# Kernel tuning notes

Hardware: AMD Instinct MI355X
Metric: run time of the kernel (lower is better)

## Reference

```python
import jax, jax.numpy as jnp
import numpy as np

DEPTH = 4
HEADS = 8
DIM = 512
HID = 1024  # int(512 * 2.0)
P = 16
IMG = 224
GRID = IMG // P          # 14
NPATCH = GRID * GRID     # 196
NTOK = NPATCH + 1        # 197 (cls token)
BATCH = 64
EPS = 1e-5               # torch LayerNorm default


def layernorm(x, w, b):
    mu = jnp.mean(x, axis=-1, keepdims=True)
    var = jnp.mean(jnp.square(x - mu), axis=-1, keepdims=True)
    return (x - mu) * jax.lax.rsqrt(var + EPS) * w + b


def setup_inputs() -> dict:
    key = jax.random.key(0)
    ks = jax.random.split(key, 12)
    s = 0.02
    inp = {
        "x": jax.random.normal(ks[0], (BATCH, 3, IMG, IMG), jnp.float32),
        # patch-embed conv as matmul: kernel flattened in torch order (c, kh, kw)
        "conv_w": jax.random.normal(ks[1], (3 * P * P, DIM), jnp.float32) * s,
        "conv_b": jnp.zeros((DIM,), jnp.float32),
        "cls_token": jax.random.normal(ks[2], (1, 1, DIM), jnp.float32) * s,
        "pos_embed": jax.random.normal(ks[3], (1, NTOK, DIM), jnp.float32) * s,
        # per-block params stacked along depth
        "ln1_w": jnp.ones((DEPTH, DIM), jnp.float32),
        "ln1_b": jnp.zeros((DEPTH, DIM), jnp.float32),
        "qkv_w": jax.random.normal(ks[4], (DEPTH, DIM, 3 * DIM), jnp.float32) * s,
        "qkv_b": jnp.zeros((DEPTH, 3 * DIM), jnp.float32),
        "proj_w": jax.random.normal(ks[5], (DEPTH, DIM, DIM), jnp.float32) * s,
        "proj_b": jnp.zeros((DEPTH, DIM), jnp.float32),
        "ln2_w": jnp.ones((DEPTH, DIM), jnp.float32),
        "ln2_b": jnp.zeros((DEPTH, DIM), jnp.float32),
        "fc1_w": jax.random.normal(ks[6], (DEPTH, DIM, HID), jnp.float32) * s,
        "fc1_b": jnp.zeros((DEPTH, HID), jnp.float32),
        "fc2_w": jax.random.normal(ks[7], (DEPTH, HID, DIM), jnp.float32) * s,
        "fc2_b": jnp.zeros((DEPTH, DIM), jnp.float32),
        "norm_w": jnp.ones((DIM,), jnp.float32),
        "norm_b": jnp.zeros((DIM,), jnp.float32),
    }
    return inp


def reference(x, conv_w, conv_b, cls_token, pos_embed,
              ln1_w, ln1_b, qkv_w, qkv_b, proj_w, proj_b,
              ln2_w, ln2_b, fc1_w, fc1_b, fc2_w, fc2_b,
              norm_w, norm_b):
    B = x.shape[0]
    hd = DIM // HEADS
    scale = hd ** -0.5
    # PatchEmbed: conv with kernel=stride=patch == patch extraction + matmul
    patches = x.reshape(B, 3, GRID, P, GRID, P)
    patches = patches.transpose(0, 2, 4, 1, 3, 5).reshape(B, NPATCH, 3 * P * P)
    tok = patches @ conv_w + conv_b                      # [B, 196, DIM]
    cls = jnp.broadcast_to(cls_token, (B, 1, DIM))
    h = jnp.concatenate([cls, tok], axis=1) + pos_embed  # [B, 197, DIM]
    for i in range(DEPTH):
        # Attention block (eval mode: dropouts are identity)
        y = layernorm(h, ln1_w[i], ln1_b[i])
        qkv = (y @ qkv_w[i] + qkv_b[i]).reshape(B, NTOK, 3, HEADS, hd)
        qkv = qkv.transpose(2, 0, 3, 1, 4)               # [3, B, H, N, hd]
        q, k, v = qkv[0], qkv[1], qkv[2]
        attn = jax.nn.softmax(jnp.einsum('bhnd,bhmd->bhnm', q, k) * scale, axis=-1)
        o = jnp.einsum('bhnm,bhmd->bhnd', attn, v)
        o = o.transpose(0, 2, 1, 3).reshape(B, NTOK, DIM)
        h = h + (o @ proj_w[i] + proj_b[i])
        # MLP block (exact GELU as in torch nn.GELU)
        y = layernorm(h, ln2_w[i], ln2_b[i])
        y = jax.nn.gelu(y @ fc1_w[i] + fc1_b[i], approximate=False)
        h = h + (y @ fc2_w[i] + fc2_b[i])
    return layernorm(h, norm_w, norm_b)
```

## Files before the change

### kernel.cpp

```cpp
#include <hip/hip_runtime.h>
#include <hip/hip_bf16.h>

#define HEADS 8
#define DIM 512
#define HID 1024
#define NTOK 197
#define NPATCH 196
#define BATCH 64
#define MTOK (BATCH*NTOK)
#define MPATCH (BATCH*NPATCH)
#define KPATCH 768

typedef __attribute__((ext_vector_type(8))) short vbf8;
typedef __attribute__((ext_vector_type(4))) float vf4;

__device__ inline float bf2f(short u) {
  union { unsigned int i; float f; } v; v.i = ((unsigned int)(unsigned short)u) << 16; return v.f;
}
__device__ inline short f2bf(float f) {
  union { float f; unsigned int i; } u; u.f = f;
  unsigned int r = u.i + 0x7fffu + ((u.i >> 16) & 1u);
  return (short)(r >> 16);
}

__device__ inline void gl_lds16(const void* g, void* l) {
  __builtin_amdgcn_global_load_lds(
      (const __attribute__((address_space(1))) void*)g,
      (__attribute__((address_space(3))) void*)l, 16, 0, 0);
}

__global__ void k_cvt_t(const float* __restrict__ in, short* __restrict__ out, int K, int N) {
  int slice = blockIdx.z;
  in  += (size_t)slice * K * N;
  out += (size_t)slice * K * N;
  __shared__ short tile[64][72];
  int t = threadIdx.x;
  int k0 = blockIdx.y * 64, n0 = blockIdx.x * 64;
  int r = t >> 2, c4 = (t & 3) << 4;
  #pragma unroll
  for (int j = 0; j < 16; j += 4) {
    float4 v = *(const float4*)(in + (size_t)(k0 + r) * N + n0 + c4 + j);
    tile[r][c4 + j + 0] = f2bf(v.x);
    tile[r][c4 + j + 1] = f2bf(v.y);
    tile[r][c4 + j + 2] = f2bf(v.z);
    tile[r][c4 + j + 3] = f2bf(v.w);
  }
  __syncthreads();
  int n = t >> 2, kc = (t & 3) << 4;
  vbf8 a, b;
  #pragma unroll
  for (int j = 0; j < 8; ++j) a[j] = tile[kc + j][n];
  #pragma unroll
  for (int j = 0; j < 8; ++j) b[j] = tile[kc + 8 + j][n];
  *(vbf8*)(out + (size_t)(n0 + n) * K + k0 + kc) = a;
  *(vbf8*)(out + (size_t)(n0 + n) * K + k0 + kc + 8) = b;
}

__global__ void k_im2col(const float* __restrict__ x, short* __restrict__ patches) {
  int tid = blockIdx.x * 256 + threadIdx.x;
  if (tid >= MPATCH * 48) return;
  int b = tid / (NPATCH * 48);
  int r = tid % (NPATCH * 48);
  int p = r / 48;
  int ck = r % 48;
  int c = ck >> 4, kh = ck & 15;
  int gy = p / 14, gx = p % 14;
  const float* src = x + ((size_t)((b * 3 + c) * 224) + gy * 16 + kh) * 224 + gx * 16;
  short* dst = patches + (size_t)(b * NPATCH + p) * KPATCH + c * 256 + kh * 16;
  float4 v0 = *(const float4*)(src);
  float4 v1 = *(const float4*)(src + 4);
  float4 v2 = *(const float4*)(src + 8);
  float4 v3 = *(const float4*)(src + 12);
  vbf8 o0, o1;
  o0[0]=f2bf(v0.x); o0[1]=f2bf(v0.y); o0[2]=f2bf(v0.z); o0[3]=f2bf(v0.w);
  o0[4]=f2bf(v1.x); o0[5]=f2bf(v1.y); o0[6]=f2bf(v1.z); o0[7]=f2bf(v1.w);
  o1[0]=f2bf(v2.x); o1[1]=f2bf(v2.y); o1[2]=f2bf(v2.z); o1[3]=f2bf(v2.w);
  o1[4]=f2bf(v3.x); o1[5]=f2bf(v3.y); o1[6]=f2bf(v3.z); o1[7]=f2bf(v3.w);
  *(vbf8*)dst = o0;
  *(vbf8*)(dst + 8) = o1;
}

__global__ void k_cls(const float* __restrict__ cls, const float* __restrict__ pos,
                      float* __restrict__ h) {
  int b = blockIdx.x, t = threadIdx.x;
  float* hr = h + (size_t)b * NTOK * DIM;
  hr[t]       = cls[t]       + pos[t];
  hr[t + 256] = cls[t + 256] + pos[t + 256];
}

template<int OUTBF>
__global__ __launch_bounds__(256) void k_ln(const float* __restrict__ x,
                                            const float* __restrict__ w,
                                            const float* __restrict__ b,
                                            void* __restrict__ out) {
  int wid = threadIdx.x >> 6, lane = threadIdx.x & 63;
  int row = blockIdx.x * 4 + wid;
  const float* xr = x + (size_t)row * DIM + lane * 8;
  float4 va = *(const float4*)xr;
  float4 vb = *(const float4*)(xr + 4);
  float s  = va.x + va.y + va.z + va.w + vb.x + vb.y + vb.z + vb.w;
  float ss = va.x*va.x + va.y*va.y + va.z*va.z + va.w*va.w
           + vb.x*vb.x + vb.y*vb.y + vb.z*vb.z + vb.w*vb.w;
  #pragma unroll
  for (int o = 32; o > 0; o >>= 1) { s += __shfl_xor(s, o); ss += __shfl_xor(ss, o); }
  float mu = s * (1.0f / DIM);
  float var = ss * (1.0f / DIM) - mu * mu;
  float rs = rsqrtf(var + 1e-5f);
  float4 wa = *(const float4*)(w + lane * 8);
  float4 wb = *(const float4*)(w + lane * 8 + 4);
  float4 ba = *(const float4*)(b + lane * 8);
  float4 bb = *(const float4*)(b + lane * 8 + 4);
  float y0 = (va.x - mu) * rs * wa.x + ba.x;
  float y1 = (va.y - mu) * rs * wa.y + ba.y;
  float y2 = (va.z - mu) * rs * wa.z + ba.z;
  float y3 = (va.w - mu) * rs * wa.w + ba.w;
  float y4 = (vb.x - mu) * rs * wb.x + bb.x;
  float y5 = (vb.y - mu) * rs * wb.y + bb.y;
  float y6 = (vb.z - mu) * rs * wb.z + bb.z;
  float y7 = (vb.w - mu) * rs * wb.w + bb.w;
  if (OUTBF) {
    vbf8 pk;
    pk[0]=f2bf(y0); pk[1]=f2bf(y1); pk[2]=f2bf(y2); pk[3]=f2bf(y3);
    pk[4]=f2bf(y4); pk[5]=f2bf(y5); pk[6]=f2bf(y6); pk[7]=f2bf(y7);
    *(vbf8*)((short*)out + (size_t)row * DIM + lane * 8) = pk;
  } else {
    float4 oa, ob;
    oa.x=y0; oa.y=y1; oa.z=y2; oa.w=y3;
    ob.x=y4; ob.y=y5; ob.z=y6; ob.w=y7;
    float* op = (float*)out + (size_t)row * DIM + lane * 8;
    *(float4*)op = oa;
    *(float4*)(op + 4) = ob;
  }
}

template<int MODE, int KU>
__global__ __launch_bounds__(256) void k_gemm(
    const short* __restrict__ A, const short* __restrict__ Bt,
    const float* __restrict__ bias, void* __restrict__ out,
    const float* __restrict__ extra, int M, int N, int K)
{
  __shared__ short As[KU][128 * 64];
  __shared__ short Bs[KU][128 * 64];
  int gx = gridDim.x;
  int nwg = gx * gridDim.y;
  int orig = blockIdx.y * gx + blockIdx.x;
  int q = nwg >> 3, r = nwg & 7, xcd = orig & 7, off = orig >> 3;
  int nid = (xcd < r ? xcd * (q + 1) : r * (q + 1) + (xcd - r) * q) + off;
  int bm = nid / gx, bn = nid % gx;

  int t = threadIdx.x, wid = t >> 6, lane = t & 63;
  int wm = wid >> 1, wn = wid & 1;
  int lr = lane & 15, lk = lane >> 4;
  int srow = lane >> 3;
  int scol = (lane & 7) * 8;
  vf4 acc[4][4];
  #pragma unroll
  for (int i = 0; i < 4; ++i)
    #pragma unroll
    for (int j = 0; j < 4; ++j) {
      acc[i][j][0] = 0.f; acc[i][j][1] = 0.f; acc[i][j][2] = 0.f; acc[i][j][3] = 0.f;
    }

  const short* Abase = A  + (size_t)(bm * 128 + srow) * K + scol;
  const short* Bbase = Bt + (size_t)(bn * 128 + srow) * K + scol;

  for (int k0 = 0; k0 < K; k0 += KU * 64) {
    if (k0) __syncthreads();
    #pragma unroll
    for (int u = 0; u < KU; ++u) {
      #pragma unroll
      for (int i = 0; i < 4; ++i) {
        int rc = wid * 4 + i;
        gl_lds16(Abase + (size_t)(rc * 8) * K + k0 + u * 64, &As[u][rc * 512]);
        gl_lds16(Bbase + (size_t)(rc * 8) * K + k0 + u * 64, &Bs[u][rc * 512]);
      }
    }
    __syncthreads();
    #pragma unroll
    for (int u = 0; u < KU; ++u) {
      #pragma unroll
      for (int s = 0; s < 2; ++s) {
        vbf8 af[4], bfr[4];
        #pragma unroll
        for (int i = 0; i < 4; ++i)
          af[i] = *(const vbf8*)&As[u][(wm * 64 + i * 16 + lr) * 64 + s * 32 + lk * 8];
        #pragma unroll
        for (int j = 0; j < 4; ++j)
          bfr[j] = *(const vbf8*)&Bs[u][(wn * 64 + j * 16 + lr) * 64 + s * 32 + lk * 8];
        #pragma unroll
        for (int i = 0; i < 4; ++i)
          #pragma unroll
          for (int j = 0; j < 4; ++j)
            acc[i][j] = __builtin_amdgcn_mfma_f32_16x16x32_bf16(af[i], bfr[j], acc[i][j], 0, 0, 0);
      }
    }
  }

  int rbase = bm * 128 + wm * 64;
  int cbase = bn * 128 + wn * 64;
  #pragma unroll
  for (int i = 0; i < 4; ++i) {
    #pragma unroll
    for (int j = 0; j < 4; ++j) {
      int col = cbase + j * 16 + lr;
      float bs = bias[col];
      #pragma unroll
      for (int z = 0; z < 4; ++z) {
        int row = rbase + i * 16 + lk * 4 + z;
        if (row < M) {
          float v = acc[i][j][z] + bs;
          if (MODE == 0) {
            ((short*)out)[(size_t)row * N + col] = f2bf(v);
          } else if (MODE == 1) {
            float g = 0.5f * v * (1.f + erff(v * 0.70710678118f));
            ((short*)out)[(size_t)row * N + col] = f2bf(g);
          } else if (MODE == 2) {
            float* hp = (float*)out + (size_t)row * N + col;
            *hp = *hp + v;
          } else {
            int b_ = row / NPATCH, p = row - b_ * NPATCH;
            ((float*)out)[((size_t)b_ * NTOK + 1 + p) * DIM + col] =
                v + extra[(size_t)(1 + p) * DIM + col];
          }
        }
      }
    }
  }
}

#define VSTR 232
__global__ __launch_bounds__(256) void k_attn(const short* __restrict__ qkv,
                                              short* __restrict__ o) {
  int h = blockIdx.x, b = blockIdx.y;
  __shared__ short Vt[64 * VSTR];
  __shared__ short Pt[4][16 * VSTR];
  int t = threadIdx.x, wid = t >> 6, lane = t & 63;
  int lq = lane & 15, g4 = lane >> 4;
  const size_t base = (size_t)(b * NTOK) * 1536 + h * 64;

  vbf8 vz;
  #pragma unroll
  for (int j = 0; j < 8; ++j) vz[j] = 0;
  for (int idx = t; idx < 224 * 8; idx += 256) {
    int r = idx >> 3, c8 = idx & 7;
    vbf8 v = vz;
    if (r < NTOK) v = *(const vbf8*)(qkv + base + (size_t)r * 1536 + 1024 + c8 * 8);
    int cs = r ^ ((c8 & 3) << 3);
    #pragma unroll
    for (int j = 0; j < 8; ++j) Vt[(c8 * 8 + j) * VSTR + cs] = v[j];
  }
  __syncthreads();

  short* Pw = &Pt[wid][0];
  for (int qt = wid; qt < 13; qt += 4) {
    const short* qp = qkv + base + (size_t)(qt * 16 + lq) * 1536 + g4 * 8;
    vbf8 qf0 = *(const vbf8*)qp;
    vbf8 qf1 = *(const vbf8*)(qp + 32);
    float sc[13][4];
    #pragma unroll
    for (int kt = 0; kt < 13; ++kt) {
      const short* kp = qkv + base + (size_t)(kt * 16 + lq) * 1536 + 512 + g4 * 8;
      vbf8 kf0 = *(const vbf8*)kp;
      vbf8 kf1 = *(const vbf8*)(kp + 32);
      vf4 s; s[0] = 0.f; s[1] = 0.f; s[2] = 0.f; s[3] = 0.f;
      s = __builtin_amdgcn_mfma_f32_16x16x32_bf16(kf0, qf0, s, 0, 0, 0);
      s = __builtin_amdgcn_mfma_f32_16x16x32_bf16(kf1, qf1, s, 0, 0, 0);
      #pragma unroll
      for (int z = 0; z < 4; ++z) {
        int krow = kt * 16 + g4 * 4 + z;
        sc[kt][z] = (krow < NTOK) ? s[z] * 0.125f : -1e30f;
      }
    }
    float mx = -1e30f;
    #pragma unroll
    for (int kt = 0; kt < 13; ++kt)
      #pragma unroll
      for (int z = 0; z < 4; ++z) mx = fmaxf(mx, sc[kt][z]);
    mx = fmaxf(mx, __shfl_xor(mx, 16));
    mx = fmaxf(mx, __shfl_xor(mx, 32));
    float sum = 0.f;
    #pragma unroll
    for (int kt = 0; kt < 13; ++kt)
      #pragma unroll
      for (int z = 0; z < 4; ++z) {
        float e = __expf(sc[kt][z] - mx);
        sc[kt][z] = e;
        sum += e;
      }
    sum += __shfl_xor(sum, 16);
    sum += __shfl_xor(sum, 32);
    float inv = 1.f / sum;
    #pragma unroll
    for (int kt = 0; kt < 13; ++kt) {
      *(short4*)&Pw[lq * VSTR + kt * 16 + g4 * 4] =
          make_short4(f2bf(sc[kt][0]), f2bf(sc[kt][1]), f2bf(sc[kt][2]), f2bf(sc[kt][3]));
    }
    *(short4*)&Pw[lq * VSTR + 208 + g4 * 4] = make_short4(0, 0, 0, 0);
    vf4 oacc[4];
    #pragma unroll
    for (int dt = 0; dt < 4; ++dt) { oacc[dt][0]=0.f; oacc[dt][1]=0.f; oacc[dt][2]=0.f; oacc[dt][3]=0.f; }
    #pragma unroll
    for (int u = 0; u < 7; ++u) {
      vbf8 pb = *(const vbf8*)&Pw[lq * VSTR + u * 32 + g4 * 8];
      #pragma unroll
      for (int dt = 0; dt < 4; ++dt) {
        int swz = ((dt * 2 + (lq >> 3)) & 3) << 3;
        vbf8 va = *(const vbf8*)&Vt[(dt * 16 + lq) * VSTR + ((u * 32 + g4 * 8) ^ swz)];
        oacc[dt] = __builtin_amdgcn_mfma_f32_16x16x32_bf16(va, pb, oacc[dt], 0, 0, 0);
      }
    }
    int qrow = qt * 16 + lq;
    if (qrow < NTOK) {
      short* op = o + ((size_t)(b * NTOK) + qrow) * DIM + h * 64 + g4 * 4;
      #pragma unroll
      for (int dt = 0; dt < 4; ++dt)
        *(short4*)(op + dt * 16) = make_short4(f2bf(oacc[dt][0] * inv), f2bf(oacc[dt][1] * inv),
                                               f2bf(oacc[dt][2] * inv), f2bf(oacc[dt][3] * inv));
    }
  }
}

extern "C" void kernel_launch(void* const* d_in, const int* in_sizes, int n_in,
                              void* d_out, int out_size, void* d_ws, size_t ws_size,
                              hipStream_t stream) {
  (void)in_sizes; (void)n_in; (void)out_size; (void)ws_size;
  const float* x      = (const float*)d_in[0];
  const float* conv_w = (const float*)d_in[1];
  const float* conv_b = (const float*)d_in[2];
  const float* cls    = (const float*)d_in[3];
  const float* pos    = (const float*)d_in[4];
  const float* ln1_w  = (const float*)d_in[5];
  const float* ln1_b  = (const float*)d_in[6];
  const float* qkv_w  = (const float*)d_in[7];
  const float* qkv_b  = (const float*)d_in[8];
  const float* proj_w = (const float*)d_in[9];
  const float* proj_b = (const float*)d_in[10];
  const float* ln2_w  = (const float*)d_in[11];
  const float* ln2_b  = (const float*)d_in[12];
  const float* fc1_w  = (const float*)d_in[13];
  const float* fc1_b  = (const float*)d_in[14];
  const float* fc2_w  = (const float*)d_in[15];
  const float* fc2_b  = (const float*)d_in[16];
  const float* norm_w = (const float*)d_in[17];
  const float* norm_b = (const float*)d_in[18];

  short* conv_wT = (short*)d_ws;
  short* qkv_wT  = conv_wT + (size_t)512 * 768;
  short* proj_wT = qkv_wT  + (size_t)4 * 1536 * 512;
  short* fc1_wT  = proj_wT + (size_t)4 * 512 * 512;
  short* fc2_wT  = fc1_wT  + (size_t)4 * 512 * 1024;
  short* y_bf    = fc2_wT  + (size_t)4 * 1024 * 512;
  short* o_bf    = y_bf    + (size_t)MTOK * 512;
  short* big     = o_bf    + (size_t)MTOK * 512;
  float* h       = (float*)(big + (size_t)MTOK * 1536);

  k_cvt_t<<<dim3(8, 12, 1), 256, 0, stream>>>(conv_w, conv_wT, 768, 512);
  k_cvt_t<<<dim3(24, 8, 4), 256, 0, stream>>>(qkv_w, qkv_wT, 512, 1536);
  k_cvt_t<<<dim3(8, 8, 4), 256, 0, stream>>>(proj_w, proj_wT, 512, 512);
  k_cvt_t<<<dim3(16, 8, 4), 256, 0, stream>>>(fc1_w, fc1_wT, 512, 1024);
  k_cvt_t<<<dim3(8, 16, 4), 256, 0, stream>>>(fc2_w, fc2_wT, 1024, 512);

  k_im2col<<<2352, 256, 0, stream>>>(x, big);
  k_cls<<<64, 256, 0, stream>>>(cls, pos, h);
  k_gemm<3, 2><<<dim3(4, 98), 256, 0, stream>>>(big, conv_wT, conv_b, h, pos,
                                                MPATCH, 512, 768);
  for (int i = 0; i < 4; ++i) {
    k_ln<1><<<MTOK / 4, 256, 0, stream>>>(h, ln1_w + i * 512, ln1_b + i * 512, y_bf);
    k_gemm<0, 2><<<dim3(12, 99), 256, 0, stream>>>(y_bf, qkv_wT + (size_t)i * 512 * 1536,
                                                   qkv_b + i * 1536, big, nullptr,
                                                   MTOK, 1536, 512);
    k_attn<<<dim3(8, 64), 256, 0, stream>>>(big, o_bf);
    k_gemm<2, 2><<<dim3(4, 99), 256, 0, stream>>>(o_bf, proj_wT + (size_t)i * 512 * 512,
                                                  proj_b + i * 512, h, nullptr,
                                                  MTOK, 512, 512);
    k_ln<1><<<MTOK / 4, 256, 0, stream>>>(h, ln2_w + i * 512, ln2_b + i * 512, y_bf);
    k_gemm<1, 2><<<dim3(8, 99), 256, 0, stream>>>(y_bf, fc1_wT + (size_t)i * 512 * 1024,
                                                  fc1_b + i * 1024, big, nullptr,
                                                  MTOK, 1024, 512);
    k_gemm<2, 2><<<dim3(4, 99), 256, 0, stream>>>(big, fc2_wT + (size_t)i * 1024 * 512,
                                                  fc2_b + i * 512, h, nullptr,
                                                  MTOK, 512, 1024);
  }
  k_ln<0><<<MTOK / 4, 256, 0, stream>>>(h, norm_w, norm_b, d_out);
}
```

Baseline: 895.5 us.

## Double-buffer GEMM LDS tiles to overlap global loads with MFMA compute

Replaces the load-all-then-compute loop over two 64-wide K slices with a ping-pong pipeline. The next K tile is staged into the alternate LDS buffer while MFMAs run on the current one, using a partial vmcnt wait and explicit barriers. The aim is to hide global-to-LDS latency behind matrix math in all GEMMs. The cost is two barriers per 64-wide K step instead of two per 128, and correctness now relies on the hand-set vmcnt count matching the eight outstanding loads.

```diff
diff --git a/kernel.cpp b/kernel.cpp
--- a/kernel.cpp
+++ b/kernel.cpp
@@ -133,14 +133,14 @@
   }
 }
 
-template<int MODE, int KU>
+template<int MODE>
 __global__ __launch_bounds__(256) void k_gemm(
     const short* __restrict__ A, const short* __restrict__ Bt,
     const float* __restrict__ bias, void* __restrict__ out,
     const float* __restrict__ extra, int M, int N, int K)
 {
-  __shared__ short As[KU][128 * 64];
-  __shared__ short Bs[KU][128 * 64];
+  __shared__ short As[2][128 * 64];
+  __shared__ short Bs[2][128 * 64];
   int gx = gridDim.x;
   int nwg = gx * gridDim.y;
   int orig = blockIdx.y * gx + blockIdx.x;
@@ -153,6 +153,19 @@
   int lr = lane & 15, lk = lane >> 4;
   int srow = lane >> 3;
   int scol = (lane & 7) * 8;
+
+  const short* Abase = A  + (size_t)(bm * 128 + srow) * K + scol;
+  const short* Bbase = Bt + (size_t)(bn * 128 + srow) * K + scol;
+
+  auto stage = [&](int buf, int k0) {
+    #pragma unroll
+    for (int i = 0; i < 4; ++i) {
+      int rc = wid * 4 + i;
+      gl_lds16(Abase + (size_t)(rc * 8) * K + k0, &As[buf][rc * 512]);
+      gl_lds16(Bbase + (size_t)(rc * 8) * K + k0, &Bs[buf][rc * 512]);
+    }
+  };
+
   vf4 acc[4][4];
   #pragma unroll
   for (int i = 0; i < 4; ++i)
@@ -161,39 +174,38 @@
       acc[i][j][0] = 0.f; acc[i][j][1] = 0.f; acc[i][j][2] = 0.f; acc[i][j][3] = 0.f;
     }
 
-  const short* Abase = A  + (size_t)(bm * 128 + srow) * K + scol;
-  const short* Bbase = Bt + (size_t)(bn * 128 + srow) * K + scol;
-
-  for (int k0 = 0; k0 < K; k0 += KU * 64) {
-    if (k0) __syncthreads();
-    #pragma unroll
-    for (int u = 0; u < KU; ++u) {
-      #pragma unroll
-      for (int i = 0; i < 4; ++i) {
-        int rc = wid * 4 + i;
-        gl_lds16(Abase + (size_t)(rc * 8) * K + k0 + u * 64, &As[u][rc * 512]);
-        gl_lds16(Bbase + (size_t)(rc * 8) * K + k0 + u * 64, &Bs[u][rc * 512]);
-      }
-    }
-    __syncthreads();
-    #pragma unroll
-    for (int u = 0; u < KU; ++u) {
-      #pragma unroll
-      for (int s = 0; s < 2; ++s) {
-        vbf8 af[4], bfr[4];
-        #pragma unroll
-        for (int i = 0; i < 4; ++i)
-          af[i] = *(const vbf8*)&As[u][(wm * 64 + i * 16 + lr) * 64 + s * 32 + lk * 8];
+  int nt = K >> 6;
+  int cur = 0;
+  stage(0, 0);
+  for (int tt = 0; tt < nt; ++tt) {
+    if (tt + 1 < nt) {
+      stage(cur ^ 1, (tt + 1) << 6);
+      asm volatile("s_waitcnt vmcnt(8)" ::: "memory");
+    } else {
+      asm volatile("s_waitcnt vmcnt(0)" ::: "memory");
+    }
+    __builtin_amdgcn_sched_barrier(0);
+    __builtin_amdgcn_s_barrier();
+    __builtin_amdgcn_sched_barrier(0);
+    #pragma unroll
+    for (int s = 0; s < 2; ++s) {
+      vbf8 af[4], bfr[4];
+      #pragma unroll
+      for (int i = 0; i < 4; ++i)
+        af[i] = *(const vbf8*)&As[cur][(wm * 64 + i * 16 + lr) * 64 + s * 32 + lk * 8];
+      #pragma unroll
+      for (int j = 0; j < 4; ++j)
+        bfr[j] = *(const vbf8*)&Bs[cur][(wn * 64 + j * 16 + lr) * 64 + s * 32 + lk * 8];
+      #pragma unroll
+      for (int i = 0; i < 4; ++i)
         #pragma unroll
         for (int j = 0; j < 4; ++j)
-          bfr[j] = *(const vbf8*)&Bs[u][(wn * 64 + j * 16 + lr) * 64 + s * 32 + lk * 8];
-        #pragma unroll
-        for (int i = 0; i < 4; ++i)
-          #pragma unroll
-          for (int j = 0; j < 4; ++j)
-            acc[i][j] = __builtin_amdgcn_mfma_f32_16x16x32_bf16(af[i], bfr[j], acc[i][j], 0, 0, 0);
-      }
-    }
+          acc[i][j] = __builtin_amdgcn_mfma_f32_16x16x32_bf16(af[i], bfr[j], acc[i][j], 0, 0, 0);
+    }
+    __builtin_amdgcn_sched_barrier(0);
+    __builtin_amdgcn_s_barrier();
+    __builtin_amdgcn_sched_barrier(0);
+    cur ^= 1;
   }
 
   int rbase = bm * 128 + wm * 64;
@@ -362,24 +374,24 @@
 
   k_im2col<<<2352, 256, 0, stream>>>(x, big);
   k_cls<<<64, 256, 0, stream>>>(cls, pos, h);
-  k_gemm<3, 2><<<dim3(4, 98), 256, 0, stream>>>(big, conv_wT, conv_b, h, pos,
-                                                MPATCH, 512, 768);
+  k_gemm<3><<<dim3(4, 98), 256, 0, stream>>>(big, conv_wT, conv_b, h, pos,
+                                             MPATCH, 512, 768);
   for (int i = 0; i < 4; ++i) {
     k_ln<1><<<MTOK / 4, 256, 0, stream>>>(h, ln1_w + i * 512, ln1_b + i * 512, y_bf);
-    k_gemm<0, 2><<<dim3(12, 99), 256, 0, stream>>>(y_bf, qkv_wT + (size_t)i * 512 * 1536,
-                                                   qkv_b + i * 1536, big, nullptr,
-                                                   MTOK, 1536, 512);
+    k_gemm<0><<<dim3(12, 99), 256, 0, stream>>>(y_bf, qkv_wT + (size_t)i * 512 * 1536,
+                                                qkv_b + i * 1536, big, nullptr,
+                                                MTOK, 1536, 512);
     k_attn<<<dim3(8, 64), 256, 0, stream>>>(big, o_bf);
-    k_gemm<2, 2><<<dim3(4, 99), 256, 0, stream>>>(o_bf, proj_wT + (size_t)i * 512 * 512,
-                                                  proj_b + i * 512, h, nullptr,
-                                                  MTOK, 512, 512);
+    k_gemm<2><<<dim3(4, 99), 256, 0, stream>>>(o_bf, proj_wT + (size_t)i * 512 * 512,
+                                               proj_b + i * 512, h, nullptr,
+                                               MTOK, 512, 512);
     k_ln<1><<<MTOK / 4, 256, 0, stream>>>(h, ln2_w + i * 512, ln2_b + i * 512, y_bf);
-    k_gemm<1, 2><<<dim3(8, 99), 256, 0, stream>>>(y_bf, fc1_wT + (size_t)i * 512 * 1024,
-                                                  fc1_b + i * 1024, big, nullptr,
-                                                  MTOK, 1024, 512);
-    k_gemm<2, 2><<<dim3(4, 99), 256, 0, stream>>>(big, fc2_wT + (size_t)i * 1024 * 512,
-                                                  fc2_b + i * 512, h, nullptr,
-                                                  MTOK, 512, 1024);
+    k_gemm<1><<<dim3(8, 99), 256, 0, stream>>>(y_bf, fc1_wT + (size_t)i * 512 * 1024,
+                                               fc1_b + i * 1024, big, nullptr,
+                                               MTOK, 1024, 512);
+    k_gemm<2><<<dim3(4, 99), 256, 0, stream>>>(big, fc2_wT + (size_t)i * 1024 * 512,
+                                               fc2_b + i * 512, h, nullptr,
+                                               MTOK, 512, 1024);
   }
   k_ln<0><<<MTOK / 4, 256, 0, stream>>>(h, norm_w, norm_b, d_out);
 }
```

Result: slower. 1.009 ms (+12.6%).
